# Optimization experiments

Hardware: AMD Instinct MI355X
Metric: run time of the kernel (lower is better)

The kernel has to match this reference:

```python
import jax, jax.numpy as jnp
import numpy as np

B, D_FEAT, D_ATTR, N_CLS = 512, 2048, 312, 150


def setup_inputs() -> dict:
    key = jax.random.key(0)
    k1, k2, k3, k4, k5 = jax.random.split(key, 5)
    return {
        "x_f": jax.random.normal(k1, (B, D_FEAT), dtype=jnp.float32),
        "W": jax.random.normal(k2, (D_FEAT, D_ATTR), dtype=jnp.float32) * 0.02,
        "b": jax.random.normal(k3, (D_ATTR,), dtype=jnp.float32) * 0.02,
        "seen_att": jax.random.normal(k4, (N_CLS, D_ATTR), dtype=jnp.float32),
        "x_labels": jax.random.randint(k5, (B,), 0, N_CLS, dtype=jnp.int64),
    }


def reference(x_f, W, b, seen_att, x_labels):
    temp = 1.0
    pre_attr = x_f @ W + b                                # [B, D]
    log_p = jax.nn.log_softmax(pre_attr / temp, axis=-1)  # log pre_attr_softmax
    log_g = jax.nn.log_softmax(seen_att[x_labels] / temp, axis=-1)
    g = jnp.exp(log_g)                                    # gt_attr_softmax [B, D]

    # pairwise KL(target = g_i/g_j || input_logits = log(p_i/p_j)), reduction='sum':
    #   sum_d t * (log t - log_ratio_p)
    t_ratio = g[:, None, :] / g[None, :, :]                               # [B, B, D]
    log_t = log_g[:, None, :] - log_g[None, :, :]                         # [B, B, D]
    log_r = log_p[:, None, :] - log_p[None, :, :]                         # [B, B, D]
    kl = jnp.sum(t_ratio * (log_t - log_r), axis=-1)                      # [B, B]

    same = x_labels[:, None] == x_labels[None, :]
    upper = jnp.triu(jnp.ones((x_labels.shape[0],) * 2, dtype=bool), k=1)
    mask = same & upper

    count = jnp.sum(mask)
    loss = jnp.sum(jnp.where(mask, kl, 0.0))
    return jnp.where(count > 0, loss / count.astype(loss.dtype), loss)
```

## Files before the change

kernel.cpp:

```cpp
#include <hip/hip_runtime.h>
#include <math.h>

#define B      512
#define DF     2048
#define DA     312
#define NTHR   320
#define RT     8
#define KSPLIT 16

__device__ __forceinline__ float wave_max_f(float v) {
  #pragma unroll
  for (int off = 32; off >= 1; off >>= 1)
    v = fmaxf(v, __shfl_down(v, off));
  return v;
}

__device__ __forceinline__ double wave_sum_d(double v) {
  #pragma unroll
  for (int off = 32; off >= 1; off >>= 1)
    v += __shfl_down(v, off);
  return v;
}

__global__ __launch_bounds__(NTHR) void gemm_partial_kernel(
    const float* __restrict__ x_f, const float* __restrict__ W,
    float* __restrict__ part, int KC) {
  const int c    = threadIdx.x;
  const int row0 = blockIdx.x * RT;
  const int k0   = blockIdx.y * KC;

  if (c >= DA) return;

  float acc[RT];
  #pragma unroll
  for (int r = 0; r < RT; ++r) acc[r] = 0.f;

  const float* Wp = W + (size_t)k0 * DA + c;
  const float* xp = x_f + (size_t)row0 * DF + k0;

  for (int k = 0; k < KC; k += 8) {
    float w[8];
    #pragma unroll
    for (int j = 0; j < 8; ++j) w[j] = Wp[(size_t)(k + j) * DA];
    #pragma unroll
    for (int r = 0; r < RT; ++r) {
      const float* xr = xp + (size_t)r * DF + k;
      #pragma unroll
      for (int j = 0; j < 8; ++j) acc[r] = fmaf(xr[j], w[j], acc[r]);
    }
  }

  #pragma unroll
  for (int r = 0; r < RT; ++r)
    part[((size_t)blockIdx.y * B + row0 + r) * DA + c] = acc[r];
}

__global__ __launch_bounds__(NTHR) void row_stats_kernel(
    const float* __restrict__ part, const float* __restrict__ b,
    double* __restrict__ S, int ksplit) {
  __shared__ float  red_f[8];
  __shared__ double red_d[16];
  __shared__ float  bcast_max;

  const int tid  = threadIdx.x;
  const int wid  = tid >> 6;
  const int lane = tid & 63;
  const int row  = blockIdx.x;

  float v = -INFINITY;
  if (tid < DA) {
    float s = b[tid];
    for (int p = 0; p < ksplit; ++p)
      s += part[((size_t)p * B + row) * DA + tid];
    v = s;
  }

  float m = wave_max_f(v);
  if (lane == 0) red_f[wid] = m;
  __syncthreads();
  if (tid == 0) {
    float mm = red_f[0];
    #pragma unroll
    for (int w = 1; w < NTHR / 64; ++w) mm = fmaxf(mm, red_f[w]);
    bcast_max = mm;
  }
  __syncthreads();
  const float rowmax = bcast_max;

  double e  = (tid < DA) ? exp((double)v - (double)rowmax) : 0.0;
  double sp = (tid < DA) ? (double)v : 0.0;
  double es = wave_sum_d(e);
  double ss = wave_sum_d(sp);
  if (lane == 0) { red_d[wid] = es; red_d[8 + wid] = ss; }
  __syncthreads();
  if (tid == 0) {
    double esum = 0.0, ssum = 0.0;
    #pragma unroll
    for (int w = 0; w < NTHR / 64; ++w) { esum += red_d[w]; ssum += red_d[8 + w]; }
    S[row] = ssum - (double)DA * ((double)rowmax + log(esum));
  }
}

__global__ __launch_bounds__(1024) void pair_reduce_kernel(
    const double* __restrict__ S, const int* __restrict__ labels,
    float* __restrict__ out) {
  __shared__ double    Ss[B];
  __shared__ int       Ls[B];
  __shared__ double    red_d[16];
  __shared__ long long red_i[16];

  const int tid = threadIdx.x;
  if (tid < B) { Ss[tid] = S[tid]; Ls[tid] = labels[tid]; }
  __syncthreads();

  double lsum = 0.0;
  long long lcnt = 0;
  for (int p = tid; p < B * B; p += 1024) {
    int i = p >> 9;
    int j = p & (B - 1);
    if (j > i && Ls[i] == Ls[j]) { lsum += Ss[j] - Ss[i]; lcnt++; }
  }

  #pragma unroll
  for (int off = 32; off >= 1; off >>= 1) {
    lsum += __shfl_down(lsum, off);
    lcnt += __shfl_down(lcnt, off);
  }
  const int wid = tid >> 6, lane = tid & 63;
  if (lane == 0) { red_d[wid] = lsum; red_i[wid] = lcnt; }
  __syncthreads();
  if (tid == 0) {
    double s = 0.0; long long c = 0;
    #pragma unroll
    for (int w = 0; w < 16; ++w) { s += red_d[w]; c += red_i[w]; }
    out[0] = (float)((c > 0) ? s / (double)c : s);
  }
}

extern "C" void kernel_launch(void* const* d_in, const int* in_sizes, int n_in,
                              void* d_out, int out_size, void* d_ws, size_t ws_size,
                              hipStream_t stream) {
  const float* x_f    = (const float*)d_in[0];
  const float* W      = (const float*)d_in[1];
  const float* b      = (const float*)d_in[2];
  const int*   labels = (const int*)d_in[4];

  int ksplit = KSPLIT;
  if (ws_size < (size_t)KSPLIT * B * DA * 4 + 8192) ksplit = 2;

  float*  part = (float*)d_ws;
  size_t  part_bytes = ((size_t)ksplit * B * DA * 4 + 255) & ~(size_t)255;
  double* S    = (double*)((char*)d_ws + part_bytes);
  const int KC = DF / ksplit;

  dim3 g1(B / RT, ksplit);
  gemm_partial_kernel<<<g1, NTHR, 0, stream>>>(x_f, W, part, KC);
  row_stats_kernel<<<B, NTHR, 0, stream>>>(part, b, S, ksplit);
  pair_reduce_kernel<<<1, 1024, 0, stream>>>(S, labels, (float*)d_out);
}
```

Measured before the change: 112.6 us.

## Fuse pair reduction into row-stats via last-block counter and raise K-split

Folds the single-block pairwise reduction into the row-stats kernel: every block publishes its row value atomically, and the last block to arrive (tracked by a global counter) computes the loss. That block replaces the O(B^2) pair loop with per-row rank counting and a weighted sum. The GEMM K-split becomes a compile-time template parameter and rises from 16 to 32 when the workspace allows, and the inner loop is widened to 16 with unroll 2. In exchange, a memset launch is added for the counter, and the partial-sum buffer grows, so row_stats reads more data.

New measurement: 139.9 us. 1.24x slower.

```diff
diff --git a/kernel.cpp b/kernel.cpp
--- a/kernel.cpp
+++ b/kernel.cpp
@@ -6,7 +6,6 @@
 #define DA     312
 #define NTHR   320
 #define RT     8
-#define KSPLIT 16
 
 __device__ __forceinline__ float wave_max_f(float v) {
   #pragma unroll
@@ -22,9 +21,11 @@
   return v;
 }
 
+template <int KSPL>
 __global__ __launch_bounds__(NTHR) void gemm_partial_kernel(
     const float* __restrict__ x_f, const float* __restrict__ W,
-    float* __restrict__ part, int KC) {
+    float* __restrict__ part) {
+  constexpr int KC = DF / KSPL;
   const int c    = threadIdx.x;
   const int row0 = blockIdx.x * RT;
   const int k0   = blockIdx.y * KC;
@@ -38,15 +39,16 @@
   const float* Wp = W + (size_t)k0 * DA + c;
   const float* xp = x_f + (size_t)row0 * DF + k0;
 
-  for (int k = 0; k < KC; k += 8) {
-    float w[8];
+  #pragma unroll 2
+  for (int k = 0; k < KC; k += 16) {
+    float w[16];
     #pragma unroll
-    for (int j = 0; j < 8; ++j) w[j] = Wp[(size_t)(k + j) * DA];
+    for (int j = 0; j < 16; ++j) w[j] = Wp[(size_t)(k + j) * DA];
     #pragma unroll
     for (int r = 0; r < RT; ++r) {
       const float* xr = xp + (size_t)r * DF + k;
       #pragma unroll
-      for (int j = 0; j < 8; ++j) acc[r] = fmaf(xr[j], w[j], acc[r]);
+      for (int j = 0; j < 16; ++j) acc[r] = fmaf(xr[j], w[j], acc[r]);
     }
   }
 
@@ -55,12 +57,18 @@
     part[((size_t)blockIdx.y * B + row0 + r) * DA + c] = acc[r];
 }
 
-__global__ __launch_bounds__(NTHR) void row_stats_kernel(
+template <int KSPL>
+__global__ __launch_bounds__(NTHR) void row_stats_fused_kernel(
     const float* __restrict__ part, const float* __restrict__ b,
-    double* __restrict__ S, int ksplit) {
+    const int* __restrict__ labels, double* __restrict__ S,
+    unsigned int* __restrict__ counter, float* __restrict__ out) {
   __shared__ float  red_f[8];
   __shared__ double red_d[16];
+  __shared__ long long red_i[8];
   __shared__ float  bcast_max;
+  __shared__ int    is_last;
+  __shared__ double Ss[B];
+  __shared__ int    Ls[B];
 
   const int tid  = threadIdx.x;
   const int wid  = tid >> 6;
@@ -70,7 +78,8 @@
   float v = -INFINITY;
   if (tid < DA) {
     float s = b[tid];
-    for (int p = 0; p < ksplit; ++p)
+    #pragma unroll
+    for (int p = 0; p < KSPL; ++p)
       s += part[((size_t)p * B + row) * DA + tid];
     v = s;
   }
@@ -97,43 +106,53 @@
     double esum = 0.0, ssum = 0.0;
     #pragma unroll
     for (int w = 0; w < NTHR / 64; ++w) { esum += red_d[w]; ssum += red_d[8 + w]; }
-    S[row] = ssum - (double)DA * ((double)rowmax + log(esum));
+    double Sv = ssum - (double)DA * ((double)rowmax + log(esum));
+    __hip_atomic_store(&S[row], Sv, __ATOMIC_RELEASE, __HIP_MEMORY_SCOPE_AGENT);
+    unsigned int old = __hip_atomic_fetch_add(counter, 1u, __ATOMIC_ACQ_REL,
+                                              __HIP_MEMORY_SCOPE_AGENT);
+    is_last = (old == B - 1) ? 1 : 0;
   }
-}
+  __syncthreads();
+  if (!is_last) return;
 
-__global__ __launch_bounds__(1024) void pair_reduce_kernel(
-    const double* __restrict__ S, const int* __restrict__ labels,
-    float* __restrict__ out) {
-  __shared__ double    Ss[B];
-  __shared__ int       Ls[B];
-  __shared__ double    red_d[16];
-  __shared__ long long red_i[16];
-
-  const int tid = threadIdx.x;
-  if (tid < B) { Ss[tid] = S[tid]; Ls[tid] = labels[tid]; }
+  for (int i = tid; i < B; i += NTHR) {
+    Ss[i] = __hip_atomic_load(&S[i], __ATOMIC_ACQUIRE, __HIP_MEMORY_SCOPE_AGENT);
+    Ls[i] = labels[i];
+  }
   __syncthreads();
 
-  double lsum = 0.0;
-  long long lcnt = 0;
-  for (int p = tid; p < B * B; p += 1024) {
-    int i = p >> 9;
-    int j = p & (B - 1);
-    if (j > i && Ls[i] == Ls[j]) { lsum += Ss[j] - Ss[i]; lcnt++; }
+  const int i0 = tid, i1 = tid + NTHR;
+  const int l0 = Ls[i0];
+  const int l1 = (i1 < B) ? Ls[i1] : -1;
+  int r0 = 0, m0 = 0, r1 = 0, m1 = 0;
+  for (int j = 0; j < B; ++j) {
+    int lj = Ls[j];
+    m0 += (lj == l0);
+    r0 += (lj == l0 && j < i0);
+    m1 += (lj == l1);
+    r1 += (lj == l1 && j < i1);
+  }
+
+  double lsum = (double)(2 * r0 - m0 + 1) * Ss[i0];
+  long long pcnt = m0 - 1;
+  if (i1 < B) {
+    lsum += (double)(2 * r1 - m1 + 1) * Ss[i1];
+    pcnt += m1 - 1;
   }
 
   #pragma unroll
   for (int off = 32; off >= 1; off >>= 1) {
     lsum += __shfl_down(lsum, off);
-    lcnt += __shfl_down(lcnt, off);
+    pcnt += __shfl_down(pcnt, off);
   }
-  const int wid = tid >> 6, lane = tid & 63;
-  if (lane == 0) { red_d[wid] = lsum; red_i[wid] = lcnt; }
+  if (lane == 0) { red_d[wid] = lsum; red_i[wid] = pcnt; }
   __syncthreads();
   if (tid == 0) {
-    double s = 0.0; long long c = 0;
+    double s = 0.0; long long c2 = 0;
     #pragma unroll
-    for (int w = 0; w < 16; ++w) { s += red_d[w]; c += red_i[w]; }
-    out[0] = (float)((c > 0) ? s / (double)c : s);
+    for (int w = 0; w < NTHR / 64; ++w) { s += red_d[w]; c2 += red_i[w]; }
+    double cnt = (double)(c2 / 2);
+    out[0] = (float)((c2 > 0) ? s / cnt : s);
   }
 }
 
@@ -145,16 +164,21 @@
   const float* b      = (const float*)d_in[2];
   const int*   labels = (const int*)d_in[4];
 
-  int ksplit = KSPLIT;
-  if (ws_size < (size_t)KSPLIT * B * DA * 4 + 8192) ksplit = 2;
+  auto launch = [&](auto ksplit_tag) {
+    constexpr int KSPL = decltype(ksplit_tag)::value;
+    float*  part = (float*)d_ws;
+    size_t  part_bytes = ((size_t)KSPL * B * DA * 4 + 255) & ~(size_t)255;
+    double* S    = (double*)((char*)d_ws + part_bytes);
+    unsigned int* counter = (unsigned int*)((char*)S + (size_t)B * 8);
 
-  float*  part = (float*)d_ws;
-  size_t  part_bytes = ((size_t)ksplit * B * DA * 4 + 255) & ~(size_t)255;
-  double* S    = (double*)((char*)d_ws + part_bytes);
-  const int KC = DF / ksplit;
+    hipMemsetAsync(counter, 0, sizeof(unsigned int), stream);
+    dim3 g1(B / RT, KSPL);
+    gemm_partial_kernel<KSPL><<<g1, NTHR, 0, stream>>>(x_f, W, part);
+    row_stats_fused_kernel<KSPL><<<B, NTHR, 0, stream>>>(part, b, labels, S,
+                                                         counter, (float*)d_out);
+  };
 
-  dim3 g1(B / RT, ksplit);
-  gemm_partial_kernel<<<g1, NTHR, 0, stream>>>(x_f, W, part, KC);
-  row_stats_kernel<<<B, NTHR, 0, stream>>>(part, b, S, ksplit);
-  pair_reduce_kernel<<<1, 1024, 0, stream>>>(S, labels, (float*)d_out);
+  const size_t need32 = ((size_t)32 * B * DA * 4 + 255 + 255) + (size_t)B * 8 + 64;
+  if (ws_size >= need32) launch(std::integral_constant<int, 32>{});
+  else                   launch(std::integral_constant<int, 4>{});
 }
```

## Use 4x4 register tiles with float4 loads in split-K GEMM

Applied to the files above, without the earlier changes.

The GEMM kernel is restructured so that each thread computes a 4-row by 4-column register tile, loading W and x with float4 instead of scalar loads. Each block now covers 16 rows instead of 8. The aim is more FMAs per loaded value and fewer memory instructions. The workspace-size fallback is removed and the split-K count becomes a compile-time constant, so the code now assumes the workspace is large enough. Threads past the last valid column reuse a clamped column and skip the store.

New measurement: 118.0 us. 1.05x slower.

```diff
diff --git a/kernel.cpp b/kernel.cpp
--- a/kernel.cpp
+++ b/kernel.cpp
@@ -5,8 +5,9 @@
 #define DF     2048
 #define DA     312
 #define NTHR   320
-#define RT     8
-#define KSPLIT 16
+#define RT     16
+#define KSPL   16
+#define KC     (DF / KSPL)
 
 __device__ __forceinline__ float wave_max_f(float v) {
   #pragma unroll
@@ -24,40 +25,70 @@
 
 __global__ __launch_bounds__(NTHR) void gemm_partial_kernel(
     const float* __restrict__ x_f, const float* __restrict__ W,
-    float* __restrict__ part, int KC) {
-  const int c    = threadIdx.x;
+    float* __restrict__ part) {
+  const int tid  = threadIdx.x;
+  const int wave = tid >> 6;
+  const int lane = tid & 63;
+  const int cg   = lane & 15;
+  const int rg   = lane >> 4;
   const int row0 = blockIdx.x * RT;
   const int k0   = blockIdx.y * KC;
 
-  if (c >= DA) return;
+  const int  cbase  = wave * 64 + cg * 4;
+  const bool cvalid = (cbase < DA);
+  const int  cw     = cvalid ? cbase : (DA - 4);
 
-  float acc[RT];
+  float4 acc[4];
   #pragma unroll
-  for (int r = 0; r < RT; ++r) acc[r] = 0.f;
+  for (int rr = 0; rr < 4; ++rr) acc[rr] = make_float4(0.f, 0.f, 0.f, 0.f);
 
-  const float* Wp = W + (size_t)k0 * DA + c;
-  const float* xp = x_f + (size_t)row0 * DF + k0;
+  const float* Wp = W + (size_t)k0 * DA + cw;
+  const float* xp = x_f + (size_t)(row0 + rg) * DF + k0;
 
-  for (int k = 0; k < KC; k += 8) {
-    float w[8];
+  #pragma unroll 2
+  for (int k = 0; k < KC; k += 4) {
+    float4 wv0 = *(const float4*)(Wp + (size_t)(k + 0) * DA);
+    float4 wv1 = *(const float4*)(Wp + (size_t)(k + 1) * DA);
+    float4 wv2 = *(const float4*)(Wp + (size_t)(k + 2) * DA);
+    float4 wv3 = *(const float4*)(Wp + (size_t)(k + 3) * DA);
+    float4 xv[4];
     #pragma unroll
-    for (int j = 0; j < 8; ++j) w[j] = Wp[(size_t)(k + j) * DA];
+    for (int rr = 0; rr < 4; ++rr)
+      xv[rr] = *(const float4*)(xp + (size_t)(4 * rr) * DF + k);
+
     #pragma unroll
-    for (int r = 0; r < RT; ++r) {
-      const float* xr = xp + (size_t)r * DF + k;
-      #pragma unroll
-      for (int j = 0; j < 8; ++j) acc[r] = fmaf(xr[j], w[j], acc[r]);
+    for (int rr = 0; rr < 4; ++rr) {
+      acc[rr].x = fmaf(xv[rr].x, wv0.x, acc[rr].x);
+      acc[rr].y = fmaf(xv[rr].x, wv0.y, acc[rr].y);
+      acc[rr].z = fmaf(xv[rr].x, wv0.z, acc[rr].z);
+      acc[rr].w = fmaf(xv[rr].x, wv0.w, acc[rr].w);
+      acc[rr].x = fmaf(xv[rr].y, wv1.x, acc[rr].x);
+      acc[rr].y = fmaf(xv[rr].y, wv1.y, acc[rr].y);
+      acc[rr].z = fmaf(xv[rr].y, wv1.z, acc[rr].z);
+      acc[rr].w = fmaf(xv[rr].y, wv1.w, acc[rr].w);
+      acc[rr].x = fmaf(xv[rr].z, wv2.x, acc[rr].x);
+      acc[rr].y = fmaf(xv[rr].z, wv2.y, acc[rr].y);
+      acc[rr].z = fmaf(xv[rr].z, wv2.z, acc[rr].z);
+      acc[rr].w = fmaf(xv[rr].z, wv2.w, acc[rr].w);
+      acc[rr].x = fmaf(xv[rr].w, wv3.x, acc[rr].x);
+      acc[rr].y = fmaf(xv[rr].w, wv3.y, acc[rr].y);
+      acc[rr].z = fmaf(xv[rr].w, wv3.z, acc[rr].z);
+      acc[rr].w = fmaf(xv[rr].w, wv3.w, acc[rr].w);
     }
   }
 
-  #pragma unroll
-  for (int r = 0; r < RT; ++r)
-    part[((size_t)blockIdx.y * B + row0 + r) * DA + c] = acc[r];
+  if (cvalid) {
+    #pragma unroll
+    for (int rr = 0; rr < 4; ++rr) {
+      const int row = row0 + rg + 4 * rr;
+      *(float4*)(part + ((size_t)blockIdx.y * B + row) * DA + cbase) = acc[rr];
+    }
+  }
 }
 
 __global__ __launch_bounds__(NTHR) void row_stats_kernel(
     const float* __restrict__ part, const float* __restrict__ b,
-    double* __restrict__ S, int ksplit) {
+    double* __restrict__ S) {
   __shared__ float  red_f[8];
   __shared__ double red_d[16];
   __shared__ float  bcast_max;
@@ -70,7 +101,8 @@
   float v = -INFINITY;
   if (tid < DA) {
     float s = b[tid];
-    for (int p = 0; p < ksplit; ++p)
+    #pragma unroll
+    for (int p = 0; p < KSPL; ++p)
       s += part[((size_t)p * B + row) * DA + tid];
     v = s;
   }
@@ -145,16 +177,12 @@
   const float* b      = (const float*)d_in[2];
   const int*   labels = (const int*)d_in[4];
 
-  int ksplit = KSPLIT;
-  if (ws_size < (size_t)KSPLIT * B * DA * 4 + 8192) ksplit = 2;
+  float*  part = (float*)d_ws;
+  size_t  part_bytes = ((size_t)KSPL * B * DA * 4 + 255) & ~(size_t)255;
+  double* S    = (double*)((char*)d_ws + part_bytes);
 
-  float*  part = (float*)d_ws;
-  size_t  part_bytes = ((size_t)ksplit * B * DA * 4 + 255) & ~(size_t)255;
-  double* S    = (double*)((char*)d_ws + part_bytes);
-  const int KC = DF / ksplit;
-
-  dim3 g1(B / RT, ksplit);
-  gemm_partial_kernel<<<g1, NTHR, 0, stream>>>(x_f, W, part, KC);
-  row_stats_kernel<<<B, NTHR, 0, stream>>>(part, b, S, ksplit);
+  dim3 g1(B / RT, KSPL);
+  gemm_partial_kernel<<<g1, NTHR, 0, stream>>>(x_f, W, part);
+  row_stats_kernel<<<B, NTHR, 0, stream>>>(part, b, S);
   pair_reduce_kernel<<<1, 1024, 0, stream>>>(S, labels, (float*)d_out);
 }
```
